# Kernel optimization log

Hardware: AMD Instinct MI355X
Metric: run time of the kernel (lower is better)

The kernel has to match this reference:

```python
import jax, jax.numpy as jnp
import numpy as np

ALPHA = 0.2  # LeakyReLU negative slope


def setup_inputs() -> dict:
    key = jax.random.key(0)
    k1, k2, k3 = jax.random.split(key, 3)
    B, N, D_in, D_out = 16, 2048, 128, 128
    x = jax.random.normal(k1, (B, N, D_in), dtype=jnp.float32)
    # xavier-uniform-ish scale for params
    W = jax.random.normal(k2, (D_in, D_out), dtype=jnp.float32) * (1.414 / np.sqrt(D_in + D_out))
    a = jax.random.normal(k3, (2 * D_out, 1), dtype=jnp.float32) * (1.414 / np.sqrt(2 * D_out + 1))
    return {"x": x, "W": W, "a": a}


def reference(x, W, a):
    # h: (B, N, D)
    h = jnp.matmul(x, W)
    D = h.shape[-1]
    # a = [a1; a2]; e[b,i,j] = leakyrelu(a1 . h_i + a2 . h_j)
    a1 = a[:D, 0]   # (D,)
    a2 = a[D:, 0]   # (D,)
    s1 = jnp.einsum('bnd,d->bn', h, a1)  # (B, N) source term
    s2 = jnp.einsum('bnd,d->bn', h, a2)  # (B, N) target term
    e = jax.nn.leaky_relu(s1[:, :, None] + s2[:, None, :], negative_slope=ALPHA)  # (B, N, N)
    attention = jax.nn.softmax(e, axis=2)
    h_prime = jnp.matmul(attention, h)  # (B, N, D)
    return jax.nn.relu(h_prime)  # concat=True -> relu
```

## Files before the change

### kernel.cpp

```cpp
#include <hip/hip_runtime.h>
#include <hip/hip_bf16.h>
#include <cstddef>

#define GAT_B 16
#define GAT_N 2048
#define GAT_D 128
#define GAT_ROWS (GAT_B * GAT_N)
#define CH 256
#define CL 8
#define GAT_ALPHA 0.2f

typedef __attribute__((ext_vector_type(8))) short short8v;
typedef __attribute__((ext_vector_type(4))) float f32x4;

__device__ __forceinline__ void cvt_hilo(float x, unsigned short& hi, unsigned short& lo) {
  union { float f; unsigned u; } a;
  a.f = x;
  hi = (unsigned short)(a.u >> 16);
  union { unsigned u; float f; } b;
  b.u = (unsigned)hi << 16;
  union { float f; unsigned u; } c;
  c.f = x - b.f;
  lo = (unsigned short)(c.u >> 16);
}

__global__ __launch_bounds__(256) void k1_gemm(const float* __restrict__ x,
                                               const float* __restrict__ W,
                                               const float* __restrict__ aa,
                                               float* __restrict__ h,
                                               float* __restrict__ s1part,
                                               float* __restrict__ s2part) {
  __shared__ unsigned short xH[64 * 128];
  __shared__ unsigned short xL[64 * 128];
  const int tid = threadIdx.x;
  const int row0 = blockIdx.x * 64;

#pragma unroll
  for (int p = 0; p < 8; ++p) {
    const int row = p * 8 + (tid >> 5);
    const int f4 = tid & 31;
    const float4 v = ((const float4*)(x + (size_t)(row0 + row) * GAT_D))[f4];
    unsigned short h0, h1, h2, h3, l0, l1, l2, l3;
    cvt_hilo(v.x, h0, l0);
    cvt_hilo(v.y, h1, l1);
    cvt_hilo(v.z, h2, l2);
    cvt_hilo(v.w, h3, l3);
    const int slot = (f4 >> 1) ^ (row & 7);
    const int base = row * 128 + slot * 8 + (f4 & 1) * 4;
    *(ushort4*)&xH[base] = make_ushort4(h0, h1, h2, h3);
    *(ushort4*)&xL[base] = make_ushort4(l0, l1, l2, l3);
  }

  const int w = tid >> 6, l = tid & 63;
  const int wc0 = w * 32;
  const int g = l >> 4, c16 = l & 15;

  short8v bh[4][2], bl[4][2];
#pragma unroll
  for (int ks = 0; ks < 4; ++ks)
#pragma unroll
    for (int nt = 0; nt < 2; ++nt) {
      const int n = wc0 + nt * 16 + c16;
#pragma unroll
      for (int j = 0; j < 8; ++j) {
        unsigned short hi, lo;
        cvt_hilo(W[(ks * 32 + g * 8 + j) * 128 + n], hi, lo);
        bh[ks][nt][j] = (short)hi;
        bl[ks][nt][j] = (short)lo;
      }
    }

  __syncthreads();

  f32x4 acc[4][2];
#pragma unroll
  for (int mt = 0; mt < 4; ++mt)
#pragma unroll
    for (int nt = 0; nt < 2; ++nt) acc[mt][nt] = (f32x4)(0.f);

#pragma unroll
  for (int ks = 0; ks < 4; ++ks) {
    short8v ah[4], al[4];
#pragma unroll
    for (int mt = 0; mt < 4; ++mt) {
      const int row = mt * 16 + c16;
      const int ai = row * 128 + (((ks * 4 + g) ^ (row & 7)) * 8);
      ah[mt] = *(const short8v*)&xH[ai];
      al[mt] = *(const short8v*)&xL[ai];
    }
#pragma unroll
    for (int mt = 0; mt < 4; ++mt) {
#pragma unroll
      for (int nt = 0; nt < 2; ++nt) {
        acc[mt][nt] = __builtin_amdgcn_mfma_f32_16x16x32_bf16(ah[mt], bh[ks][nt], acc[mt][nt], 0, 0, 0);
        acc[mt][nt] = __builtin_amdgcn_mfma_f32_16x16x32_bf16(al[mt], bh[ks][nt], acc[mt][nt], 0, 0, 0);
        acc[mt][nt] = __builtin_amdgcn_mfma_f32_16x16x32_bf16(ah[mt], bl[ks][nt], acc[mt][nt], 0, 0, 0);
      }
    }
  }

#pragma unroll
  for (int mt = 0; mt < 4; ++mt)
#pragma unroll
    for (int nt = 0; nt < 2; ++nt)
#pragma unroll
      for (int j = 0; j < 4; ++j)
        h[(size_t)(row0 + mt * 16 + g * 4 + j) * GAT_D + wc0 + nt * 16 + c16] =
            acc[mt][nt][j];

  float a1v[2], a2v[2];
#pragma unroll
  for (int nt = 0; nt < 2; ++nt) {
    a1v[nt] = aa[wc0 + nt * 16 + c16];
    a2v[nt] = aa[128 + wc0 + nt * 16 + c16];
  }
#pragma unroll
  for (int mt = 0; mt < 4; ++mt) {
#pragma unroll
    for (int j = 0; j < 4; ++j) {
      float t1 = acc[mt][0][j] * a1v[0] + acc[mt][1][j] * a1v[1];
      float t2 = acc[mt][0][j] * a2v[0] + acc[mt][1][j] * a2v[1];
#pragma unroll
      for (int off = 1; off < 16; off <<= 1) {
        t1 += __shfl_xor(t1, off);
        t2 += __shfl_xor(t2, off);
      }
      if (c16 == 0) {
        const int row = row0 + mt * 16 + g * 4 + j;
        s1part[w * GAT_ROWS + row] = t1;
        s2part[w * GAT_ROWS + row] = t2;
      }
    }
  }
}

__global__ __launch_bounds__(1024) void k2_sort(const float* __restrict__ s1part,
                                                const float* __restrict__ s2part,
                                                int* __restrict__ idxs,
                                                int* __restrict__ rids,
                                                float* __restrict__ wA,
                                                float* __restrict__ wP,
                                                int* __restrict__ pNat,
                                                float* __restrict__ c1,
                                                float* __restrict__ c2) {
  __shared__ float v[2048];
  __shared__ int id[2048];
  __shared__ float denA[2048];
  __shared__ float denP[2048];
  __shared__ float wtotA[16];
  __shared__ float wtotP[16];
  const int tid = threadIdx.x;
  const int b = blockIdx.x >> 1;
  const int half = blockIdx.x & 1;
  const int i0 = tid, i1 = tid + 1024;
  const float* src = (half == 0) ? s2part : s1part;
  {
    const int r0 = b * GAT_N + i0, r1 = b * GAT_N + i1;
    float v0 = src[r0] + src[GAT_ROWS + r0] + src[2 * GAT_ROWS + r0] + src[3 * GAT_ROWS + r0];
    float v1 = src[r1] + src[GAT_ROWS + r1] + src[2 * GAT_ROWS + r1] + src[3 * GAT_ROWS + r1];
    if (half == 1) {
      v0 = -v0;
      v1 = -v1;
    }
    v[i0] = v0;
    v[i1] = v1;
  }
  __syncthreads();

  const int lane = tid & 63;
  const int e0 = ((tid >> 6) << 7) + lane * 2;
  const int e1 = e0 + 1;
  float va = v[e0], vb = v[e1];
  int ida = e0, idb = e1;

  auto lanex = [&](int k, int j) {
    const int jl = j >> 1;
    const bool dir = (e0 & k) == 0;
    const bool lower = (lane & jl) == 0;
    const bool keepMax = lower ^ dir;
    {
      const float ov = __shfl_xor(va, jl);
      const int oid = __shfl_xor(ida, jl);
      const bool ogt = (ov > va) || (ov == va && oid > ida);
      if (ogt == keepMax) { va = ov; ida = oid; }
    }
    {
      const float ov = __shfl_xor(vb, jl);
      const int oid = __shfl_xor(idb, jl);
      const bool ogt = (ov > vb) || (ov == vb && oid > idb);
      if (ogt == keepMax) { vb = ov; idb = oid; }
    }
  };
  auto pairx = [&](int k) {
    const bool dir = (e0 & k) == 0;
    const bool bgt = (vb > va) || (vb == va && idb > ida);
    if (bgt != dir) {
      const float tv = va; va = vb; vb = tv;
      const int ti = ida; ida = idb; idb = ti;
    }
  };

#pragma unroll
  for (int k = 2; k <= 128; k <<= 1) {
#pragma unroll
    for (int j = k >> 1; j >= 2; j >>= 1) lanex(k, j);
    pairx(k);
  }
  v[e0] = va; id[e0] = ida;
  v[e1] = vb; id[e1] = idb;
  __syncthreads();

  for (int k = 256; k <= 2048; k <<= 1) {
    for (int j = k >> 1; j >= 128; j >>= 1) {
      const int i = ((tid & ~(j - 1)) << 1) | (tid & (j - 1));
      const int ixj = i | j;
      const bool up = (i & k) == 0;
      const float x0 = v[i], x1 = v[ixj];
      if (up ? (x0 > x1) : (x0 < x1)) {
        v[i] = x1;
        v[ixj] = x0;
        const int ti = id[i];
        id[i] = id[ixj];
        id[ixj] = ti;
      }
      __syncthreads();
    }
    va = v[e0]; ida = id[e0];
    vb = v[e1]; idb = id[e1];
#pragma unroll
    for (int j = 64; j >= 2; j >>= 1) lanex(k, j);
    pairx(k);
    v[e0] = va; id[e0] = ida;
    v[e1] = vb; id[e1] = idb;
    __syncthreads();
  }

  if (half == 1) {
    rids[b * GAT_N + i0] = id[i0];
    rids[b * GAT_N + i1] = id[i1];
    return;
  }
  idxs[b * GAT_N + i0] = id[i0];
  idxs[b * GAT_N + i1] = id[i1];

  const int w = tid >> 6;
  const float aL = __expf(GAT_ALPHA * v[2 * tid]);
  const float aR = __expf(GAT_ALPHA * v[2 * tid + 1]);
  const float pL = __expf(v[2047 - 2 * tid]);
  const float pR = __expf(v[2046 - 2 * tid]);
  wA[b * GAT_N + 2 * tid] = aL;
  wA[b * GAT_N + 2 * tid + 1] = aR;
  wP[b * GAT_N + 2047 - 2 * tid] = pL;
  wP[b * GAT_N + 2046 - 2 * tid] = pR;
  float sA = aL + aR, sP = pL + pR;
#pragma unroll
  for (int off = 1; off < 64; off <<= 1) {
    const float tA = __shfl_up(sA, off);
    const float tP = __shfl_up(sP, off);
    if (lane >= off) {
      sA += tA;
      sP += tP;
    }
  }
  if (lane == 63) {
    wtotA[w] = sA;
    wtotP[w] = sP;
  }
  __syncthreads();
  float offA = 0.f, offP = 0.f;
  for (int ww = 0; ww < w; ++ww) {
    offA += wtotA[ww];
    offP += wtotP[ww];
  }
  const float inclA = offA + sA;
  const float inclP = offP + sP;
  denA[2 * tid] = inclA - aR;
  denA[2 * tid + 1] = inclA;
  denP[2047 - 2 * tid] = inclP - pR;
  denP[2046 - 2 * tid] = inclP;
  __syncthreads();

#pragma unroll
  for (int rr = 0; rr < 2; ++rr) {
    const int j = tid + rr * 1024;
    const int r = b * GAT_N + j;
    const float s1v = s1part[r] + s1part[GAT_ROWS + r] + s1part[2 * GAT_ROWS + r] +
                      s1part[3 * GAT_ROWS + r];
    const float tt = -s1v;
    int lo = 0, hi = GAT_N;
    while (lo < hi) {
      const int mid = (lo + hi) >> 1;
      if (v[mid] < tt)
        lo = mid + 1;
      else
        hi = mid;
    }
    const float e1 = __expf(s1v), e2 = __expf(GAT_ALPHA * s1v);
    float den = 0.f;
    if (lo < GAT_N) den += e1 * denP[lo];
    if (lo > 0) den += e2 * denA[lo - 1];
    const float inv = 1.f / den;
    pNat[r] = lo;
    c1[r] = e1 * inv;
    c2[r] = e2 * inv;
  }
}

__global__ __launch_bounds__(128) void k3_permute(const float* __restrict__ h,
                                                  const int* __restrict__ idxs,
                                                  const float* __restrict__ wA,
                                                  const float* __restrict__ wP,
                                                  float* __restrict__ hs,
                                                  float* __restrict__ partA,
                                                  float* __restrict__ partP) {
  const int b = blockIdx.x >> 7, cc = blockIdx.x & 127;
  const int d = threadIdx.x;
  const int* idxb = idxs + b * GAT_N;
  const float* hb = h + (size_t)b * GAT_N * GAT_D;
#pragma unroll
  for (int sub = 0; sub < 2; ++sub) {
    const int c = cc * 2 + sub;
    const int q0 = c * CL;
    float accA = 0.f, accP = 0.f;
#pragma unroll
    for (int qq = 0; qq < CL; ++qq) {
      const int q = q0 + qq;
      const int j = idxb[q];
      const float hv = hb[(size_t)j * GAT_D + d];
      hs[((size_t)b * GAT_N + q) * GAT_D + d] = hv;
      accA = fmaf(wA[b * GAT_N + q], hv, accA);
      accP = fmaf(wP[b * GAT_N + q], hv, accP);
    }
    partA[(b * CH + c) * GAT_D + d] = accA;
    partP[(b * CH + c) * GAT_D + d] = accP;
  }
}

__global__ __launch_bounds__(1024) void k3b_scan(const float* __restrict__ partA,
                                                 const float* __restrict__ partP,
                                                 float* __restrict__ baseA,
                                                 float* __restrict__ baseP) {
  __shared__ float totA[8][128];
  __shared__ float totP[8][128];
  const int b = blockIdx.x;
  const int t = threadIdx.x;
  const int d = t & 127, g = t >> 7;
  const float* pA = partA + (size_t)(b * CH + g * 32) * GAT_D + d;
  const float* pP = partP + (size_t)(b * CH + g * 32) * GAT_D + d;
  float sA = 0.f, sP = 0.f;
#pragma unroll 8
  for (int i = 0; i < 32; ++i) {
    sA += pA[i * GAT_D];
    sP += pP[i * GAT_D];
  }
  totA[g][d] = sA;
  totP[g][d] = sP;
  __syncthreads();
  float offA = 0.f, offP = 0.f;
  for (int gg = 0; gg < g; ++gg) offA += totA[gg][d];
  for (int gg = g + 1; gg < 8; ++gg) offP += totP[gg][d];
  float run = offA;
#pragma unroll 8
  for (int i = 0; i < 32; ++i) {
    baseA[(size_t)(b * (CH + 1) + g * 32 + i) * GAT_D + d] = run;
    run += pA[i * GAT_D];
  }
  if (g == 7) baseA[(size_t)(b * (CH + 1) + CH) * GAT_D + d] = run;
  run = offP;
#pragma unroll 8
  for (int i = 31; i >= 0; --i) {
    baseP[(size_t)(b * CH + g * 32 + i) * GAT_D + d] = run;
    run += pP[i * GAT_D];
  }
}

__global__ __launch_bounds__(512) void k5_out(const float* __restrict__ hs,
                                              const float* __restrict__ wA,
                                              const float* __restrict__ wP,
                                              const float* __restrict__ baseA,
                                              const float* __restrict__ baseP,
                                              const int* __restrict__ pNat,
                                              const float* __restrict__ c1,
                                              const float* __restrict__ c2,
                                              const int* __restrict__ rids,
                                              float* __restrict__ out) {
  const int wave = threadIdx.x >> 6, lane = threadIdx.x & 63;
  const int j = blockIdx.x * 8 + wave;
  const int b = j >> 11;
  const int jr = b * GAT_N + (j & 2047);
  const int rid = rids[jr];
  const int nr = b * GAT_N + rid;
  const int p = pNat[nr];
  const float cc1 = c1[nr], cc2 = c2[nr];
  const float2* hs2 = (const float2*)(hs + (size_t)b * GAT_N * GAT_D);
  const float* wAb = wA + b * GAT_N;
  const float* wPb = wP + b * GAT_N;

  const int cA = p >> 3;
  float2 accA = ((const float2*)(baseA + (size_t)(b * (CH + 1) + cA) * GAT_D))[lane];
#pragma unroll 4
  for (int q = cA * CL; q < p; ++q) {
    const float w = wAb[q];
    const float2 hv = hs2[(size_t)q * 64 + lane];
    accA.x = fmaf(w, hv.x, accA.x);
    accA.y = fmaf(w, hv.y, accA.y);
  }

  const int pP = p < GAT_N ? p : GAT_N - 1;
  const int cP = pP >> 3;
  float2 accP = ((const float2*)(baseP + (size_t)(b * CH + cP) * GAT_D))[lane];
  const int qend = cP * CL + CL;
#pragma unroll 4
  for (int q = p; q < qend; ++q) {
    const float w = wPb[q];
    const float2 hv = hs2[(size_t)q * 64 + lane];
    accP.x = fmaf(w, hv.x, accP.x);
    accP.y = fmaf(w, hv.y, accP.y);
  }

  const float vx = cc2 * accA.x + cc1 * accP.x;
  const float vy = cc2 * accA.y + cc1 * accP.y;
  ((float2*)out)[(size_t)nr * 64 + lane] =
      make_float2(fmaxf(vx, 0.f), fmaxf(vy, 0.f));
}

extern "C" void kernel_launch(void* const* d_in, const int* in_sizes, int n_in,
                              void* d_out, int out_size, void* d_ws, size_t ws_size,
                              hipStream_t stream) {
  (void)in_sizes;
  (void)n_in;
  (void)out_size;
  (void)ws_size;
  const float* x = (const float*)d_in[0];
  const float* W = (const float*)d_in[1];
  const float* a = (const float*)d_in[2];
  float* out = (float*)d_out;
  float* wsf = (float*)d_ws;

  const size_t HN = (size_t)GAT_ROWS * GAT_D;
  size_t o = 0;
  float* s1part = wsf + o;   o += 4 * GAT_ROWS;
  float* s2part = wsf + o;   o += 4 * GAT_ROWS;
  int* idxs = (int*)(wsf + o); o += GAT_ROWS;
  int* rids = (int*)(wsf + o); o += GAT_ROWS;
  float* wAr = wsf + o;      o += GAT_ROWS;
  float* wPr = wsf + o;      o += GAT_ROWS;
  int* pNat = (int*)(wsf + o); o += GAT_ROWS;
  float* c1 = wsf + o;       o += GAT_ROWS;
  float* c2 = wsf + o;       o += GAT_ROWS;
  float* partA = wsf + o;    o += (size_t)GAT_B * CH * GAT_D;
  float* partP = wsf + o;    o += (size_t)GAT_B * CH * GAT_D;
  float* baseA = wsf + o;    o += (size_t)GAT_B * (CH + 1) * GAT_D;
  float* baseP = wsf + o;    o += (size_t)GAT_B * CH * GAT_D;
  float* h = wsf + o;        o += HN;
  float* hs = wsf + o;       o += HN;

  k1_gemm<<<512, 256, 0, stream>>>(x, W, a, h, s1part, s2part);
  k2_sort<<<2 * GAT_B, 1024, 0, stream>>>(s1part, s2part, idxs, rids, wAr, wPr,
                                          pNat, c1, c2);
  k3_permute<<<GAT_B * 128, 128, 0, stream>>>(h, idxs, wAr, wPr, hs, partA, partP);
  k3b_scan<<<GAT_B, 1024, 0, stream>>>(partA, partP, baseA, baseP);
  k5_out<<<GAT_ROWS / 8, 512, 0, stream>>>(hs, wAr, wPr, baseA, baseP, pNat, c1, c2,
                                           rids, out);
}
```

Before: 71.31 us.

## Fuse prefix-scan into permute kernel via last-block atomic counter

```diff
diff --git a/kernel.cpp b/kernel.cpp
--- a/kernel.cpp
+++ b/kernel.cpp
@@ -312,69 +312,68 @@
                                                   const float* __restrict__ wP,
                                                   float* __restrict__ hs,
                                                   float* __restrict__ partA,
-                                                  float* __restrict__ partP) {
+                                                  float* __restrict__ partP,
+                                                  float* __restrict__ baseA,
+                                                  float* __restrict__ baseP,
+                                                  unsigned* __restrict__ counters) {
   const int b = blockIdx.x >> 7, cc = blockIdx.x & 127;
-  const int d = threadIdx.x;
+  const int t = threadIdx.x;
+  const int w = t >> 6, l = t & 63;
+  const int c = cc * 2 + w;
+  const int q0 = c * CL;
   const int* idxb = idxs + b * GAT_N;
-  const float* hb = h + (size_t)b * GAT_N * GAT_D;
-#pragma unroll
-  for (int sub = 0; sub < 2; ++sub) {
-    const int c = cc * 2 + sub;
-    const int q0 = c * CL;
-    float accA = 0.f, accP = 0.f;
-#pragma unroll
-    for (int qq = 0; qq < CL; ++qq) {
-      const int q = q0 + qq;
-      const int j = idxb[q];
-      const float hv = hb[(size_t)j * GAT_D + d];
-      hs[((size_t)b * GAT_N + q) * GAT_D + d] = hv;
-      accA = fmaf(wA[b * GAT_N + q], hv, accA);
-      accP = fmaf(wP[b * GAT_N + q], hv, accP);
-    }
-    partA[(b * CH + c) * GAT_D + d] = accA;
-    partP[(b * CH + c) * GAT_D + d] = accP;
-  }
-}
-
-__global__ __launch_bounds__(1024) void k3b_scan(const float* __restrict__ partA,
-                                                 const float* __restrict__ partP,
-                                                 float* __restrict__ baseA,
-                                                 float* __restrict__ baseP) {
-  __shared__ float totA[8][128];
-  __shared__ float totP[8][128];
-  const int b = blockIdx.x;
-  const int t = threadIdx.x;
-  const int d = t & 127, g = t >> 7;
-  const float* pA = partA + (size_t)(b * CH + g * 32) * GAT_D + d;
-  const float* pP = partP + (size_t)(b * CH + g * 32) * GAT_D + d;
-  float sA = 0.f, sP = 0.f;
+  const float2* hb2 = (const float2*)(h + (size_t)b * GAT_N * GAT_D);
+  float2* hs2 = (float2*)(hs + (size_t)b * GAT_N * GAT_D);
+  float2 accA = make_float2(0.f, 0.f), accP = make_float2(0.f, 0.f);
+#pragma unroll
+  for (int qq = 0; qq < CL; ++qq) {
+    const int q = q0 + qq;
+    const int j = idxb[q];
+    const float2 hv = hb2[(size_t)j * 64 + l];
+    hs2[(size_t)q * 64 + l] = hv;
+    const float wa = wA[b * GAT_N + q];
+    const float wp = wP[b * GAT_N + q];
+    accA.x = fmaf(wa, hv.x, accA.x);
+    accA.y = fmaf(wa, hv.y, accA.y);
+    accP.x = fmaf(wp, hv.x, accP.x);
+    accP.y = fmaf(wp, hv.y, accP.y);
+  }
+  ((float2*)partA)[(size_t)(b * CH + c) * 64 + l] = accA;
+  ((float2*)partP)[(size_t)(b * CH + c) * 64 + l] = accP;
+
+  __threadfence();
+  __shared__ int lastFlag;
+  if (t == 0) lastFlag = (atomicAdd(&counters[b], 1u) == 127u) ? 1 : 0;
+  __syncthreads();
+  if (!lastFlag) return;
+  __threadfence();
+  const float2* pA2 = (const float2*)partA + (size_t)b * CH * 64;
+  const float2* pP2 = (const float2*)partP + (size_t)b * CH * 64;
+  float2* bA2 = (float2*)baseA + (size_t)b * (CH + 1) * 64;
+  float2* bP2 = (float2*)baseP + (size_t)b * CH * 64;
+  if (w == 0) {
+    float2 run = make_float2(0.f, 0.f);
 #pragma unroll 8
-  for (int i = 0; i < 32; ++i) {
-    sA += pA[i * GAT_D];
-    sP += pP[i * GAT_D];
-  }
-  totA[g][d] = sA;
-  totP[g][d] = sP;
-  __syncthreads();
-  float offA = 0.f, offP = 0.f;
-  for (int gg = 0; gg < g; ++gg) offA += totA[gg][d];
-  for (int gg = g + 1; gg < 8; ++gg) offP += totP[gg][d];
-  float run = offA;
+    for (int ci = 0; ci < CH; ++ci) {
+      bA2[(size_t)ci * 64 + l] = run;
+      const float2 p = pA2[(size_t)ci * 64 + l];
+      run.x += p.x;
+      run.y += p.y;
+    }
+    bA2[(size_t)CH * 64 + l] = run;
+  } else {
+    float2 run = make_float2(0.f, 0.f);
 #pragma unroll 8
-  for (int i = 0; i < 32; ++i) {
-    baseA[(size_t)(b * (CH + 1) + g * 32 + i) * GAT_D + d] = run;
-    run += pA[i * GAT_D];
-  }
-  if (g == 7) baseA[(size_t)(b * (CH + 1) + CH) * GAT_D + d] = run;
-  run = offP;
-#pragma unroll 8
-  for (int i = 31; i >= 0; --i) {
-    baseP[(size_t)(b * CH + g * 32 + i) * GAT_D + d] = run;
-    run += pP[i * GAT_D];
-  }
-}
-
-__global__ __launch_bounds__(512) void k5_out(const float* __restrict__ hs,
+    for (int ci = CH - 1; ci >= 0; --ci) {
+      bP2[(size_t)ci * 64 + l] = run;
+      const float2 p = pP2[(size_t)ci * 64 + l];
+      run.x += p.x;
+      run.y += p.y;
+    }
+  }
+}
+
+__global__ __launch_bounds__(256) void k5_out(const float* __restrict__ hs,
                                               const float* __restrict__ wA,
                                               const float* __restrict__ wP,
                                               const float* __restrict__ baseA,
@@ -385,7 +384,7 @@
                                               const int* __restrict__ rids,
                                               float* __restrict__ out) {
   const int wave = threadIdx.x >> 6, lane = threadIdx.x & 63;
-  const int j = blockIdx.x * 8 + wave;
+  const int j = blockIdx.x * 4 + wave;
   const int b = j >> 11;
   const int jr = b * GAT_N + (j & 2047);
   const int rid = rids[jr];
@@ -452,14 +451,16 @@
   float* partP = wsf + o;    o += (size_t)GAT_B * CH * GAT_D;
   float* baseA = wsf + o;    o += (size_t)GAT_B * (CH + 1) * GAT_D;
   float* baseP = wsf + o;    o += (size_t)GAT_B * CH * GAT_D;
+  unsigned* counters = (unsigned*)(wsf + o); o += 16;
   float* h = wsf + o;        o += HN;
   float* hs = wsf + o;       o += HN;
 
+  hipMemsetAsync(counters, 0, GAT_B * sizeof(unsigned), stream);
   k1_gemm<<<512, 256, 0, stream>>>(x, W, a, h, s1part, s2part);
   k2_sort<<<2 * GAT_B, 1024, 0, stream>>>(s1part, s2part, idxs, rids, wAr, wPr,
                                           pNat, c1, c2);
-  k3_permute<<<GAT_B * 128, 128, 0, stream>>>(h, idxs, wAr, wPr, hs, partA, partP);
-  k3b_scan<<<GAT_B, 1024, 0, stream>>>(partA, partP, baseA, baseP);
-  k5_out<<<GAT_ROWS / 8, 512, 0, stream>>>(hs, wAr, wPr, baseA, baseP, pNat, c1, c2,
+  k3_permute<<<GAT_B * 128, 128, 0, stream>>>(h, idxs, wAr, wPr, hs, partA, partP,
+                                              baseA, baseP, counters);
+  k5_out<<<GAT_ROWS / 4, 256, 0, stream>>>(hs, wAr, wPr, baseA, baseP, pNat, c1, c2,
                                            rids, out);
 }
```

After: 236.2 us. 231% more time.
